# Kernel tuning notes

Hardware: AMD Instinct MI355X
Metric: run time of the kernel (lower is better)

The kernel has to match this reference:

```python
import jax, jax.numpy as jnp
import numpy as np

K = 15
LAM = 1.0
EPS = 1e-8


def _pdist(a):
    # pairwise euclidean distance (torch.cdist p=2), safe sqrt (zero grad at 0)
    sq = jnp.sum(a * a, axis=1)
    d2 = sq[:, None] + sq[None, :] - 2.0 * (a @ a.T)
    d2 = jnp.maximum(d2, 0.0)
    pos = d2 > 0
    return jnp.where(pos, jnp.sqrt(jnp.where(pos, d2, 1.0)), 0.0)


def _knn_distance_loss(z, xf, k):
    B = xf.shape[0]
    x_dist = _pdist(xf)
    z_dist = _pdist(z)
    eye = jnp.eye(B, dtype=bool)
    x_noself = jnp.where(eye, jnp.inf, x_dist)
    # k smallest per row -> top_k of negated distances
    _, knn_idx = jax.lax.top_k(-x_noself, k)          # (B, k)
    rows = jnp.arange(B)[:, None]
    mask = jnp.zeros((B, B), dtype=bool).at[rows, knn_idx].set(True)
    mask = mask | mask.T                              # symmetric kNN mask
    x_m = jnp.where(mask, x_dist, 0.0)
    z_m = jnp.where(mask, z_dist, 0.0)
    x_norm = x_m / (jnp.max(x_m) + EPS)
    z_norm = z_m / (jnp.max(z_m) + EPS)
    diff2 = jnp.where(mask, (z_norm - x_norm) ** 2, 0.0)
    return diff2.sum() / mask.sum().astype(diff2.dtype)


def _forward(x, We1, be1, We2, be2, Wd1, bd1, Wd2, bd2):
    h = jax.nn.relu(x @ We1 + be1)
    z = h @ We2 + be2                                  # (B, latent)
    h2 = jax.nn.relu(z @ Wd1 + bd1)
    x_rec = h2 @ Wd2 + bd2
    rec_loss = jnp.mean((x_rec - x) ** 2)
    dist_loss = _knn_distance_loss(z, x.reshape(x.shape[0], -1), K)
    return rec_loss + LAM * dist_loss


def setup_inputs() -> dict:
    key = jax.random.key(0)
    ks = jax.random.split(key, 5)
    B, D, H, L = 8192, 1024, 512, 64
    s = 0.02
    return {
        "x": jax.random.normal(ks[0], (B, D), dtype=jnp.float32),
        "We1": jax.random.normal(ks[1], (D, H), dtype=jnp.float32) * s,
        "be1": jnp.zeros((H,), dtype=jnp.float32),
        "We2": jax.random.normal(ks[2], (H, L), dtype=jnp.float32) * s,
        "be2": jnp.zeros((L,), dtype=jnp.float32),
        "Wd1": jax.random.normal(ks[3], (L, H), dtype=jnp.float32) * s,
        "bd1": jnp.zeros((H,), dtype=jnp.float32),
        "Wd2": jax.random.normal(ks[4], (H, D), dtype=jnp.float32) * s,
        "bd2": jnp.zeros((D,), dtype=jnp.float32),
    }


def reference(x, We1, be1, We2, be2, Wd1, bd1, Wd2, bd2):
    return _forward(x, We1, be1, We2, be2, Wd1, bd1, Wd2, bd2)
```

## Files before the change

### kernel.cpp

```cpp
#include <hip/hip_runtime.h>

#define BB 8192
#define DD 1024
#define HH 512
#define LL 64
#define KNN 15
#define NT 64
#define NTILES 2080
#define NG1 256
#define NEDGE (BB * KNN)
#define NEBLK (NEDGE / 128)

typedef __attribute__((ext_vector_type(4))) float f32x4;
typedef __attribute__((ext_vector_type(8))) short s16x8;
typedef __attribute__((ext_vector_type(8))) unsigned short u16x8;
typedef __attribute__((ext_vector_type(4))) unsigned short u16x4;
typedef __attribute__((ext_vector_type(4))) _Float16 f16x4;

typedef s16x8 fragT;

__device__ __forceinline__ unsigned short f2bf(float f) {
  unsigned u = __float_as_uint(f);
  return (unsigned short)((u + 0x7fffu + ((u >> 16) & 1u)) >> 16);
}

__device__ __forceinline__ void gload16(const void* g, void* l) {
  __builtin_amdgcn_global_load_lds((const __attribute__((address_space(1))) unsigned int*)g,
                                   (__attribute__((address_space(3))) unsigned int*)l, 16, 0, 0);
}

__device__ __forceinline__ float unpack_d2(unsigned u) {
  _Float16 h = __builtin_bit_cast(_Float16, (unsigned short)(u >> 16));
  return (float)h;
}

__device__ __forceinline__ void ins15(unsigned (&l)[KNN], unsigned u) {
  if (u < l[KNN - 1]) {
    unsigned v = u;
#pragma unroll
    for (int p = 0; p < KNN; ++p) {
      unsigned lo = min(v, l[p]);
      unsigned hi = max(v, l[p]);
      l[p] = lo;
      v = hi;
    }
  }
}

__global__ void k_prep(const float* __restrict__ x, unsigned short* __restrict__ xb,
                       float* __restrict__ sqx,
                       const float* __restrict__ We1, const float* __restrict__ We2,
                       const float* __restrict__ Wd1, const float* __restrict__ Wd2,
                       unsigned short* __restrict__ Wt1, unsigned short* __restrict__ Wt2,
                       unsigned short* __restrict__ Wt3, unsigned short* __restrict__ Wt4) {
  __shared__ float ps[4];
  __shared__ unsigned short T[64][65];
  int b = blockIdx.x;
  int t = threadIdx.x;
  if (b < BB) {
    f32x4 v = *(const f32x4*)(x + (size_t)b * DD + t * 4);
    u16x4 o;
    float s = 0.f;
#pragma unroll
    for (int j = 0; j < 4; ++j) {
      float f = v[j];
      s += f * f;
      o[j] = f2bf(f);
    }
    *(u16x4*)(xb + (size_t)b * DD + t * 4) = o;
#pragma unroll
    for (int off = 32; off >= 1; off >>= 1) s += __shfl_down(s, off);
    if ((t & 63) == 0) ps[t >> 6] = s;
    __syncthreads();
    if (t == 0) sqx[b] = ps[0] + ps[1] + ps[2] + ps[3];
    return;
  }
  int c = b - BB;
  const float* W;
  unsigned short* Wt;
  int Kd, N, idx;
  if (c < 128)      { W = We1; Wt = Wt1; Kd = DD; N = HH; idx = c; }
  else if (c < 136) { W = We2; Wt = Wt2; Kd = HH; N = LL; idx = c - 128; }
  else if (c < 144) { W = Wd1; Wt = Wt3; Kd = LL; N = HH; idx = c - 136; }
  else              { W = Wd2; Wt = Wt4; Kd = HH; N = DD; idx = c - 144; }
  int nx = Kd >> 6;
  int k0 = (idx % nx) * 64, n0 = (idx / nx) * 64;
  int kr = t >> 4, nc = (t & 15) * 4;
#pragma unroll
  for (int q = 0; q < 4; ++q) {
    int k = kr + q * 16;
    f32x4 v = *(const f32x4*)(W + (size_t)(k0 + k) * N + n0 + nc);
#pragma unroll
    for (int j = 0; j < 4; ++j) T[nc + j][k] = f2bf(v[j]);
  }
  __syncthreads();
#pragma unroll
  for (int q = 0; q < 2; ++q) {
    int s = t + q * 256;
    int n = s >> 3, cc = (s & 7) * 8;
    u16x8 o;
#pragma unroll
    for (int j = 0; j < 8; ++j) o[j] = T[n][cc + j];
    *(u16x8*)(Wt + (size_t)(n0 + n) * Kd + k0 + cc) = o;
  }
}

template <int NF, int RELU, int FUSE, int STF32, int STBF>
__device__ __forceinline__ void mgemm_body(
    char* LB, int m0, int n0,
    const unsigned short* __restrict__ A, const unsigned short* __restrict__ Wt,
    const float* __restrict__ bias, unsigned short* __restrict__ Cb, float* __restrict__ Cf,
    const float* __restrict__ Xref, float* __restrict__ rec_sum, int N, int Kd) {
  unsigned short* At = (unsigned short*)LB;
  unsigned short* Bt = (unsigned short*)(LB + 16384);
  int t = threadIdx.x;
  int lane = t & 63, w = t >> 6;
  int wr = w >> 1, wc = w & 1;
  int wbase = w * 64;

  const unsigned short* pA[4];
  const unsigned short* pB[NF];
#pragma unroll
  for (int q = 0; q < 4; ++q) {
    int s = q * 256 + t;
    int r = s >> 3, g = s & 7;
    pA[q] = A + (size_t)(m0 + r) * Kd + (g ^ (r & 7)) * 8;
  }
#pragma unroll
  for (int q = 0; q < NF; ++q) {
    int s = q * 256 + t;
    int r = s >> 3, g = s & 7;
    pB[q] = Wt + (size_t)(n0 + r) * Kd + (g ^ (r & 7)) * 8;
  }

  int lrow = lane & 15;
  int klo = (lane >> 4) << 4;
  int sw = (lane & 7) << 4;

  f32x4 acc[4][NF] = {};

  int ksteps = Kd >> 6;
#pragma unroll
  for (int q = 0; q < 4; ++q) { gload16(pA[q], At + (q * 256 + wbase) * 8); pA[q] += 64; }
#pragma unroll
  for (int q = 0; q < NF; ++q) { gload16(pB[q], Bt + (q * 256 + wbase) * 8); pB[q] += 64; }

  for (int kt = 0; kt < ksteps; ++kt) {
    __syncthreads();
    fragT af[2][4], bf[2][NF];
#pragma unroll
    for (int kh = 0; kh < 2; ++kh) {
      int kbyte = ((kh << 6) | klo) ^ sw;
#pragma unroll
      for (int m = 0; m < 4; ++m)
        af[kh][m] = *(const fragT*)((const char*)At + (wr * 64 + m * 16 + lrow) * 128 + kbyte);
#pragma unroll
      for (int n = 0; n < NF; ++n)
        bf[kh][n] = *(const fragT*)((const char*)Bt + (wc * NF * 16 + n * 16 + lrow) * 128 + kbyte);
    }
    __syncthreads();
    if (kt + 1 < ksteps) {
#pragma unroll
      for (int q = 0; q < 4; ++q) { gload16(pA[q], At + (q * 256 + wbase) * 8); pA[q] += 64; }
#pragma unroll
      for (int q = 0; q < NF; ++q) { gload16(pB[q], Bt + (q * 256 + wbase) * 8); pB[q] += 64; }
    }
#pragma unroll
    for (int kh = 0; kh < 2; ++kh)
#pragma unroll
      for (int m = 0; m < 4; ++m)
#pragma unroll
        for (int n = 0; n < NF; ++n)
          acc[m][n] =
              __builtin_amdgcn_mfma_f32_16x16x32_bf16(af[kh][m], bf[kh][n], acc[m][n], 0, 0, 0);
  }

  float local = 0.f;
#pragma unroll
  for (int m = 0; m < 4; ++m) {
    int row0 = m0 + wr * 64 + m * 16 + ((lane >> 4) << 2);
#pragma unroll
    for (int n = 0; n < NF; ++n) {
      int col = n0 + wc * NF * 16 + n * 16 + lrow;
      float bv = bias[col];
      f32x4 a = acc[m][n];
#pragma unroll
      for (int j = 0; j < 4; ++j) {
        float c = a[j] + bv;
        if (RELU) c = fmaxf(c, 0.f);
        if (FUSE) {
          float xv = Xref[(size_t)(row0 + j) * N + col];
          float d = c - xv;
          local = fmaf(d, d, local);
        }
        if (STBF) Cb[(size_t)(row0 + j) * N + col] = f2bf(c);
        if (STF32) Cf[(size_t)(row0 + j) * N + col] = c;
      }
    }
  }
  if (FUSE) {
#pragma unroll
    for (int off = 32; off >= 1; off >>= 1) local += __shfl_down(local, off);
    __shared__ float rs[4];
    if ((t & 63) == 0) rs[t >> 6] = local;
    __syncthreads();
    if (t == 0) atomicAdd(rec_sum, rs[0] + rs[1] + rs[2] + rs[3]);
  }
}

template <int NF, int RELU, int FUSE, int STF32, int STBF>
__global__ __launch_bounds__(256) void k_mgemm(
    const unsigned short* __restrict__ A, const unsigned short* __restrict__ Wt,
    const float* __restrict__ bias, unsigned short* __restrict__ Cb, float* __restrict__ Cf,
    const float* __restrict__ Xref, float* __restrict__ rec_sum, int N, int Kd) {
  __shared__ __attribute__((aligned(16))) char LB[16384 + NF * 32 * 128];
  mgemm_body<NF, RELU, FUSE, STF32, STBF>(LB, blockIdx.y * 128, blockIdx.x * (NF * 32),
                                          A, Wt, bias, Cb, Cf, Xref, rec_sum, N, Kd);
}

__global__ __launch_bounds__(256, 3) void k_gram_topk(
    const unsigned short* __restrict__ xb, const float* __restrict__ sqx,
    unsigned* __restrict__ part,
    const unsigned short* __restrict__ Wt1, const float* __restrict__ be1,
    unsigned short* __restrict__ hb) {
  __shared__ __attribute__((aligned(16))) char LB[33792];

  int bid0 = blockIdx.x;
  if (bid0 < NG1) {
    mgemm_body<4, 1, 0, 0, 1>(LB, (bid0 >> 2) * 128, (bid0 & 3) * 128,
                              xb, Wt1, be1, hb, nullptr, nullptr, nullptr, HH, DD);
    return;
  }

  unsigned short* At = (unsigned short*)LB;
  unsigned short* Bt = (unsigned short*)(LB + 16384);
  char* Sf = LB;
  unsigned* scratch = (unsigned*)(LB + 16384);
  float* sqr = (float*)(LB + 32768);
  float* sqc = (float*)(LB + 33280);

  int g = bid0 - NG1;
  int k = g & 7, m = g >> 3;
  int nA = 6 + 4 * (61 - 4 * k);
  int b, mm;
  if (m < nA) { b = k; mm = m; }
  else        { b = 15 - k; mm = m - nA; }
  int ctl, j;
  if (mm < 6) {
    if (mm < 1)      { ctl = 0; j = mm; }
    else if (mm < 3) { ctl = 1; j = mm - 1; }
    else             { ctl = 2; j = mm - 3; }
  } else {
    ctl = 3 + ((mm - 6) >> 2);
    j = (mm - 6) & 3;
  }
  int rt = 4 * b + j;
  int ct = 4 * b + ctl;
  bool diag = (rt == ct);
  int r0 = rt * 128, c0 = ct * 128;

  int t = threadIdx.x;
  int lane = t & 63, w = t >> 6;
  int wr = w >> 1, wc = w & 1;
  int wbase = w * 64;

  if (t < 128) {
    sqr[t] = sqx[r0 + t];
    sqc[t] = sqx[c0 + t];
  }

  const unsigned short* pA[4];
  const unsigned short* pB[4];
#pragma unroll
  for (int q = 0; q < 4; ++q) {
    int s = q * 256 + t;
    int r = s >> 3, gg = s & 7;
    int kk = (gg ^ (r & 7)) * 8;
    pA[q] = xb + (size_t)(r0 + r) * DD + kk;
    pB[q] = xb + (size_t)(c0 + r) * DD + kk;
  }

  int lrow = lane & 15;
  int klo = (lane >> 4) << 4;
  int sw = (lane & 7) << 4;

  f32x4 acc[16] = {};

#pragma unroll
  for (int q = 0; q < 4; ++q) {
    gload16(pA[q], At + (q * 256 + wbase) * 8); pA[q] += 64;
    gload16(pB[q], Bt + (q * 256 + wbase) * 8); pB[q] += 64;
  }

  for (int kt = 0; kt < 16; ++kt) {
    __syncthreads();
    fragT af[2][4], bf[2][4];
#pragma unroll
    for (int kh = 0; kh < 2; ++kh) {
      int kbyte = ((kh << 6) | klo) ^ sw;
#pragma unroll
      for (int mq = 0; mq < 4; ++mq)
        af[kh][mq] = *(const fragT*)((const char*)At + (wr * 64 + mq * 16 + lrow) * 128 + kbyte);
#pragma unroll
      for (int n = 0; n < 4; ++n)
        bf[kh][n] = *(const fragT*)((const char*)Bt + (wc * 64 + n * 16 + lrow) * 128 + kbyte);
    }
    __syncthreads();
    if (kt < 15) {
#pragma unroll
      for (int q = 0; q < 4; ++q) {
        gload16(pA[q], At + (q * 256 + wbase) * 8); pA[q] += 64;
        gload16(pB[q], Bt + (q * 256 + wbase) * 8); pB[q] += 64;
      }
    }
#pragma unroll
    for (int kh = 0; kh < 2; ++kh)
#pragma unroll
      for (int mq = 0; mq < 4; ++mq)
#pragma unroll
        for (int n = 0; n < 4; ++n)
          acc[mq * 4 + n] = __builtin_amdgcn_mfma_f32_16x16x32_bf16(af[kh][mq], bf[kh][n],
                                                                   acc[mq * 4 + n], 0, 0, 0);
  }

  unsigned rowlist[KNN];
#pragma unroll
  for (int p = 0; p < KNN; ++p) rowlist[p] = 0xFFFFFFFFu;

  int scanrow = t & 127, side = t >> 7;

#pragma unroll
  for (int nh = 0; nh < 2; ++nh) {
    if (wc == nh) {
#pragma unroll
      for (int mq = 0; mq < 4; ++mq) {
        int row0 = wr * 64 + mq * 16 + ((lane >> 4) << 2);
        f32x4 sq4 = *(const f32x4*)&sqr[row0];
#pragma unroll
        for (int n = 0; n < 4; ++n) {
          int colL = n * 16 + lrow;
          float sc = sqc[nh * 64 + colL];
          f32x4 a = acc[mq * 4 + n];
          f16x4 hv;
#pragma unroll
          for (int r = 0; r < 4; ++r) {
            float d2 = fmaxf(sq4[r] + sc - 2.f * a[r], 0.f);
            if (diag && (row0 + r == nh * 64 + colL)) d2 = 60000.f;
            hv[r] = (_Float16)d2;
          }
          *(f16x4*)(Sf + colL * 256 + (((row0 * 2)) ^ ((colL & 31) << 3))) = hv;
        }
      }
    }
    __syncthreads();
    {
      int cbase = side * 32;
      int jbase = c0 + nh * 64;
      for (int cc = 0; cc < 32; cc += 4) {
        unsigned u[4];
#pragma unroll
        for (int q = 0; q < 4; ++q) {
          int colL = cbase + cc + q;
          unsigned bits = *(const unsigned short*)(Sf + colL * 256 +
                                                   ((scanrow * 2) ^ ((colL & 31) << 3)));
          u[q] = (bits << 16) | (unsigned)(jbase + colL);
        }
        unsigned m4 = min(min(u[0], u[1]), min(u[2], u[3]));
        if (m4 < rowlist[KNN - 1]) {
#pragma unroll
          for (int q = 0; q < 4; ++q) ins15(rowlist, u[q]);
        }
      }
    }
    if (!diag) {
      int c = t & 63, seg = t >> 6;
      unsigned collist[KNN];
#pragma unroll
      for (int p = 0; p < KNN; ++p) collist[p] = 0xFFFFFFFFu;
      for (int rq = 0; rq < 8; ++rq) {
        int r = seg * 32 + rq * 4;
        u16x4 v4 = *(const u16x4*)(Sf + c * 256 + ((r * 2) ^ ((c & 31) << 3)));
        unsigned u[4];
#pragma unroll
        for (int jj = 0; jj < 4; ++jj) u[jj] = ((unsigned)v4[jj] << 16) | (unsigned)(r0 + r + jj);
        unsigned m4 = min(min(u[0], u[1]), min(u[2], u[3]));
        if (m4 < collist[KNN - 1]) {
#pragma unroll
          for (int jj = 0; jj < 4; ++jj) ins15(collist, u[jj]);
        }
      }
      __syncthreads();
#pragma unroll
      for (int p = 0; p < KNN; ++p) scratch[(c * 4 + seg) * KNN + p] = collist[p];
      __syncthreads();
      if (t < 64) {
        unsigned fin[KNN];
#pragma unroll
        for (int p = 0; p < KNN; ++p) fin[p] = 0xFFFFFFFFu;
        for (int s = 0; s < 4; ++s)
#pragma unroll
          for (int p = 0; p < KNN; ++p) ins15(fin, scratch[(t * 4 + s) * KNN + p]);
        int jj = c0 + nh * 64 + t;
#pragma unroll
        for (int p = 0; p < KNN; ++p) part[((size_t)(rt * KNN + p)) * BB + jj] = fin[p];
      }
    }
    __syncthreads();
  }

#pragma unroll
  for (int p = 0; p < KNN; ++p) scratch[(scanrow * 2 + side) * KNN + p] = rowlist[p];
  __syncthreads();
  if (t < 128) {
    unsigned fin[KNN];
#pragma unroll
    for (int p = 0; p < KNN; ++p) fin[p] = 0xFFFFFFFFu;
    for (int s = 0; s < 2; ++s)
#pragma unroll
      for (int p = 0; p < KNN; ++p) ins15(fin, scratch[(t * 2 + s) * KNN + p]);
    int i = r0 + t;
#pragma unroll
    for (int p = 0; p < KNN; ++p) part[((size_t)(ct * KNN + p)) * BB + i] = fin[p];
  }
}

__global__ void k_merge1(const unsigned* __restrict__ part, unsigned* __restrict__ part2) {
  int gid = blockIdx.x * 256 + threadIdx.x;
  int s = gid >> 13, i = gid & 8191;
  unsigned l[KNN];
#pragma unroll
  for (int p = 0; p < KNN; ++p) l[p] = 0xFFFFFFFFu;
  for (int b = s * 16; b < s * 16 + 16; ++b) {
    size_t base = (size_t)(b * KNN) * BB + i;
    unsigned u = part[base];
    if (u < l[KNN - 1]) {
      ins15(l, u);
      for (int p = 1; p < KNN; ++p) {
        u = part[base + (size_t)p * BB];
        if (u >= l[KNN - 1]) break;
        ins15(l, u);
      }
    }
  }
#pragma unroll
  for (int p = 0; p < KNN; ++p) part2[((size_t)(s * KNN + p)) * BB + i] = l[p];
}

__global__ void k_merge2(const unsigned* __restrict__ part2, float* __restrict__ knn_d2,
                         int* __restrict__ knn_idx, int* __restrict__ xmax_bits) {
  int i = blockIdx.x * 256 + threadIdx.x;
  unsigned l[KNN];
#pragma unroll
  for (int p = 0; p < KNN; ++p) l[p] = 0xFFFFFFFFu;
  for (int q = 0; q < 4; ++q) {
    size_t base = (size_t)(q * KNN) * BB + i;
    unsigned u = part2[base];
    if (u < l[KNN - 1]) {
      ins15(l, u);
      for (int p = 1; p < KNN; ++p) {
        u = part2[base + (size_t)p * BB];
        if (u >= l[KNN - 1]) break;
        ins15(l, u);
      }
    }
  }
  float mx = 0.f;
#pragma unroll
  for (int p = 0; p < KNN; ++p) {
    unsigned u = l[p];
    float d = fmaxf(unpack_d2(u), 0.f);
    mx = fmaxf(mx, d);
    knn_d2[(size_t)i * KNN + p] = d;
    knn_idx[(size_t)i * KNN + p] = (int)(u & 0xFFFFu);
  }
  int t = threadIdx.x;
#pragma unroll
  for (int off = 32; off >= 1; off >>= 1) mx = fmaxf(mx, __shfl_down(mx, off));
  __shared__ float rm[4];
  if ((t & 63) == 0) rm[t >> 6] = mx;
  __syncthreads();
  if (t == 0) {
    float mb = fmaxf(fmaxf(rm[0], rm[1]), fmaxf(rm[2], rm[3]));
    atomicMax(xmax_bits, __float_as_int(mb));
  }
}

__global__ void k_edge(const float* __restrict__ z, const int* __restrict__ knn_idx,
                       const float* __restrict__ knn_d2, float* __restrict__ pzz,
                       float* __restrict__ pxx, float* __restrict__ pxz,
                       float* __restrict__ pcnt, float* __restrict__ pzm) {
  int t = threadIdx.x;
  int g = t >> 4, L = t & 15;
  int lane = t & 63;
  float szz = 0.f, sxx = 0.f, sxz = 0.f, scnt = 0.f, zm = 0.f;
#pragma unroll
  for (int pass = 0; pass < 8; ++pass) {
    int e = blockIdx.x * 128 + pass * 16 + g;
    int i = e / KNN;
    int j = knn_idx[e];
    f32x4 zi = *(const f32x4*)(z + (size_t)i * LL + L * 4);
    f32x4 zj = *(const f32x4*)(z + (size_t)j * LL + L * 4);
    float v = 0.f;
#pragma unroll
    for (int d = 0; d < 4; ++d) {
      float df = zi[d] - zj[d];
      v = fmaf(df, df, v);
    }
    v += __shfl_down(v, 8);
    v += __shfl_down(v, 4);
    v += __shfl_down(v, 2);
    v += __shfl_down(v, 1);
    int cand = (L < KNN) ? knn_idx[(size_t)j * KNN + L] : -1;
    unsigned long long ball = __ballot(cand == i);
    unsigned recip = (unsigned)(ball >> (lane & 48)) & 0xFFFFu;
    if (L == 0) {
      float w = recip ? 1.f : 2.f;
      float xd2 = knn_d2[e];
      szz = fmaf(w, v, szz);
      sxx = fmaf(w, xd2, sxx);
      sxz = fmaf(w, sqrtf(v * xd2), sxz);
      scnt += w;
      zm = fmaxf(zm, v);
    }
  }
#pragma unroll
  for (int off = 32; off >= 1; off >>= 1) {
    szz += __shfl_down(szz, off);
    sxx += __shfl_down(sxx, off);
    sxz += __shfl_down(sxz, off);
    scnt += __shfl_down(scnt, off);
    zm = fmaxf(zm, __shfl_down(zm, off));
  }
  __shared__ float r[5][4];
  int w4 = t >> 6;
  if (lane == 0) {
    r[0][w4] = szz; r[1][w4] = sxx; r[2][w4] = sxz; r[3][w4] = scnt; r[4][w4] = zm;
  }
  __syncthreads();
  if (t == 0) {
    pzz[blockIdx.x] = r[0][0] + r[0][1] + r[0][2] + r[0][3];
    pxx[blockIdx.x] = r[1][0] + r[1][1] + r[1][2] + r[1][3];
    pxz[blockIdx.x] = r[2][0] + r[2][1] + r[2][2] + r[2][3];
    pcnt[blockIdx.x] = r[3][0] + r[3][1] + r[3][2] + r[3][3];
    pzm[blockIdx.x] = fmaxf(fmaxf(r[4][0], r[4][1]), fmaxf(r[4][2], r[4][3]));
  }
}

__global__ void k_final(const float* __restrict__ pzz, const float* __restrict__ pxx,
                        const float* __restrict__ pxz, const float* __restrict__ pcnt,
                        const float* __restrict__ pzm, const int* __restrict__ xmax_bits,
                        const float* __restrict__ rec_sum, float* __restrict__ out) {
  int t = threadIdx.x;
  float szz = 0.f, sxx = 0.f, sxz = 0.f, scnt = 0.f, zm = 0.f;
  for (int bb = t; bb < NEBLK; bb += 256) {
    szz += pzz[bb];
    sxx += pxx[bb];
    sxz += pxz[bb];
    scnt += pcnt[bb];
    zm = fmaxf(zm, pzm[bb]);
  }
#pragma unroll
  for (int off = 32; off >= 1; off >>= 1) {
    szz += __shfl_down(szz, off);
    sxx += __shfl_down(sxx, off);
    sxz += __shfl_down(sxz, off);
    scnt += __shfl_down(scnt, off);
    zm = fmaxf(zm, __shfl_down(zm, off));
  }
  __shared__ float r[5][4];
  int w4 = t >> 6;
  if ((t & 63) == 0) {
    r[0][w4] = szz; r[1][w4] = sxx; r[2][w4] = sxz; r[3][w4] = scnt; r[4][w4] = zm;
  }
  __syncthreads();
  if (t == 0) {
    float SZZ = r[0][0] + r[0][1] + r[0][2] + r[0][3];
    float SXX = r[1][0] + r[1][1] + r[1][2] + r[1][3];
    float SXZ = r[2][0] + r[2][1] + r[2][2] + r[2][3];
    float CNT = r[3][0] + r[3][1] + r[3][2] + r[3][3];
    float ZM = fmaxf(fmaxf(r[4][0], r[4][1]), fmaxf(r[4][2], r[4][3]));
    float xmax = __int_as_float(*xmax_bits);
    float a = 1.f / (sqrtf(ZM) + 1e-8f);
    float bq = 1.f / (sqrtf(xmax) + 1e-8f);
    float loss = (a * a * SZZ + bq * bq * SXX - 2.f * a * bq * SXZ) / CNT;
    out[0] = rec_sum[0] * (1.f / 8388608.f) + loss;
  }
}

extern "C" void kernel_launch(void* const* d_in, const int* in_sizes, int n_in,
                              void* d_out, int out_size, void* d_ws, size_t ws_size,
                              hipStream_t stream) {
  const float* x = (const float*)d_in[0];
  const float* We1 = (const float*)d_in[1];
  const float* be1 = (const float*)d_in[2];
  const float* We2 = (const float*)d_in[3];
  const float* be2 = (const float*)d_in[4];
  const float* Wd1 = (const float*)d_in[5];
  const float* bd1 = (const float*)d_in[6];
  const float* Wd2 = (const float*)d_in[7];
  const float* bd2 = (const float*)d_in[8];

  char* ws = (char*)d_ws;
  size_t off = 0;
  auto alloc = [&](size_t bytes) {
    void* p = ws + off;
    off += (bytes + 255) & ~(size_t)255;
    return p;
  };
  unsigned short* xb = (unsigned short*)alloc((size_t)BB * DD * 2);
  unsigned short* hb = (unsigned short*)alloc((size_t)BB * HH * 2);
  unsigned short* zb = (unsigned short*)alloc((size_t)BB * LL * 2);
  unsigned short* h2b = (unsigned short*)alloc((size_t)BB * HH * 2);
  float* z = (float*)alloc((size_t)BB * LL * 4);
  float* sqx = (float*)alloc((size_t)BB * 4);
  unsigned short* Wt1 = (unsigned short*)alloc((size_t)HH * DD * 2);
  unsigned short* Wt2 = (unsigned short*)alloc((size_t)LL * HH * 2);
  unsigned short* Wt3 = (unsigned short*)alloc((size_t)HH * LL * 2);
  unsigned short* Wt4 = (unsigned short*)alloc((size_t)DD * HH * 2);
  unsigned* part = (unsigned*)alloc((size_t)NT * KNN * BB * 4);
  unsigned* part2 = (unsigned*)alloc((size_t)4 * KNN * BB * 4);
  float* knn_d2 = (float*)alloc((size_t)BB * KNN * 4);
  int* knn_idx = (int*)alloc((size_t)BB * KNN * 4);
  float* pzz = (float*)alloc(NEBLK * 4);
  float* pxx = (float*)alloc(NEBLK * 4);
  float* pxz = (float*)alloc(NEBLK * 4);
  float* pcnt = (float*)alloc(NEBLK * 4);
  float* pzm = (float*)alloc(NEBLK * 4);
  float* scal = (float*)alloc(64);
  float* rec_sum = scal + 0;
  int* xmax_bits = (int*)(scal + 1);

  hipMemsetAsync(scal, 0, 64, stream);

  k_prep<<<BB + 272, 256, 0, stream>>>(x, xb, sqx, We1, We2, Wd1, Wd2, Wt1, Wt2, Wt3, Wt4);

  k_gram_topk<<<NG1 + NTILES, 256, 0, stream>>>(xb, sqx, part, Wt1, be1, hb);

  k_mgemm<2, 0, 0, 1, 1><<<dim3(LL / 64, BB / 128), 256, 0, stream>>>(
      hb, Wt2, be2, zb, z, nullptr, nullptr, LL, HH);
  k_mgemm<4, 1, 0, 0, 1><<<dim3(HH / 128, BB / 128), 256, 0, stream>>>(
      zb, Wt3, bd1, h2b, nullptr, nullptr, nullptr, HH, LL);
  k_mgemm<4, 0, 1, 0, 0><<<dim3(DD / 128, BB / 128), 256, 0, stream>>>(
      h2b, Wt4, bd2, nullptr, nullptr, x, rec_sum, DD, HH);

  k_merge1<<<128, 256, 0, stream>>>(part, part2);
  k_merge2<<<BB / 256, 256, 0, stream>>>(part2, knn_d2, knn_idx, xmax_bits);
  k_edge<<<NEBLK, 256, 0, stream>>>(z, knn_idx, knn_d2, pzz, pxx, pxz, pcnt, pzm);
  k_final<<<1, 256, 0, stream>>>(pzz, pxx, pxz, pcnt, pzm, xmax_bits, rec_sum, (float*)d_out);
}
```

Measured before the change: 321.5 us.

## Co-schedule tail GEMMs with kNN merge and edge kernels in combined launches

Six sequential tail kernels become three combined launches. Each launch pairs a decoder/latent GEMM with the independent kNN stage (merge1, merge2, edge) by splitting on block index, so the small merge and edge stages overlap with GEMM blocks. This removes three kernel launches and their serialization gaps. The cost is larger shared memory per block for the merge and edge blocks, and branch-divergent kernels whose occupancy is set by the GEMM path.

```diff
diff --git a/kernel.cpp b/kernel.cpp
--- a/kernel.cpp
+++ b/kernel.cpp
@@ -208,16 +208,6 @@
   }
 }
 
-template <int NF, int RELU, int FUSE, int STF32, int STBF>
-__global__ __launch_bounds__(256) void k_mgemm(
-    const unsigned short* __restrict__ A, const unsigned short* __restrict__ Wt,
-    const float* __restrict__ bias, unsigned short* __restrict__ Cb, float* __restrict__ Cf,
-    const float* __restrict__ Xref, float* __restrict__ rec_sum, int N, int Kd) {
-  __shared__ __attribute__((aligned(16))) char LB[16384 + NF * 32 * 128];
-  mgemm_body<NF, RELU, FUSE, STF32, STBF>(LB, blockIdx.y * 128, blockIdx.x * (NF * 32),
-                                          A, Wt, bias, Cb, Cf, Xref, rec_sum, N, Kd);
-}
-
 __global__ __launch_bounds__(256, 3) void k_gram_topk(
     const unsigned short* __restrict__ xb, const float* __restrict__ sqx,
     unsigned* __restrict__ part,
@@ -424,8 +414,8 @@
   }
 }
 
-__global__ void k_merge1(const unsigned* __restrict__ part, unsigned* __restrict__ part2) {
-  int gid = blockIdx.x * 256 + threadIdx.x;
+__device__ __forceinline__ void merge1_body(int gid, const unsigned* __restrict__ part,
+                                            unsigned* __restrict__ part2) {
   int s = gid >> 13, i = gid & 8191;
   unsigned l[KNN];
 #pragma unroll
@@ -446,9 +436,9 @@
   for (int p = 0; p < KNN; ++p) part2[((size_t)(s * KNN + p)) * BB + i] = l[p];
 }
 
-__global__ void k_merge2(const unsigned* __restrict__ part2, float* __restrict__ knn_d2,
-                         int* __restrict__ knn_idx, int* __restrict__ xmax_bits) {
-  int i = blockIdx.x * 256 + threadIdx.x;
+__device__ __forceinline__ void merge2_body(int i, const unsigned* __restrict__ part2,
+                                            float* __restrict__ knn_d2, int* __restrict__ knn_idx,
+                                            int* __restrict__ xmax_bits) {
   unsigned l[KNN];
 #pragma unroll
   for (int p = 0; p < KNN; ++p) l[p] = 0xFFFFFFFFu;
@@ -485,17 +475,19 @@
   }
 }
 
-__global__ void k_edge(const float* __restrict__ z, const int* __restrict__ knn_idx,
-                       const float* __restrict__ knn_d2, float* __restrict__ pzz,
-                       float* __restrict__ pxx, float* __restrict__ pxz,
-                       float* __restrict__ pcnt, float* __restrict__ pzm) {
+__device__ __forceinline__ void edge_body(int eb, const float* __restrict__ z,
+                                          const int* __restrict__ knn_idx,
+                                          const float* __restrict__ knn_d2,
+                                          float* __restrict__ pzz, float* __restrict__ pxx,
+                                          float* __restrict__ pxz, float* __restrict__ pcnt,
+                                          float* __restrict__ pzm) {
   int t = threadIdx.x;
   int g = t >> 4, L = t & 15;
   int lane = t & 63;
   float szz = 0.f, sxx = 0.f, sxz = 0.f, scnt = 0.f, zm = 0.f;
 #pragma unroll
   for (int pass = 0; pass < 8; ++pass) {
-    int e = blockIdx.x * 128 + pass * 16 + g;
+    int e = eb * 128 + pass * 16 + g;
     int i = e / KNN;
     int j = knn_idx[e];
     f32x4 zi = *(const f32x4*)(z + (size_t)i * LL + L * 4);
@@ -538,11 +530,55 @@
   }
   __syncthreads();
   if (t == 0) {
-    pzz[blockIdx.x] = r[0][0] + r[0][1] + r[0][2] + r[0][3];
-    pxx[blockIdx.x] = r[1][0] + r[1][1] + r[1][2] + r[1][3];
-    pxz[blockIdx.x] = r[2][0] + r[2][1] + r[2][2] + r[2][3];
-    pcnt[blockIdx.x] = r[3][0] + r[3][1] + r[3][2] + r[3][3];
-    pzm[blockIdx.x] = fmaxf(fmaxf(r[4][0], r[4][1]), fmaxf(r[4][2], r[4][3]));
+    pzz[eb] = r[0][0] + r[0][1] + r[0][2] + r[0][3];
+    pxx[eb] = r[1][0] + r[1][1] + r[1][2] + r[1][3];
+    pxz[eb] = r[2][0] + r[2][1] + r[2][2] + r[2][3];
+    pcnt[eb] = r[3][0] + r[3][1] + r[3][2] + r[3][3];
+    pzm[eb] = fmaxf(fmaxf(r[4][0], r[4][1]), fmaxf(r[4][2], r[4][3]));
+  }
+}
+
+__global__ __launch_bounds__(256) void k_tail2(
+    const unsigned short* __restrict__ hb, const unsigned short* __restrict__ Wt2,
+    const float* __restrict__ be2, unsigned short* __restrict__ zb, float* __restrict__ z,
+    const unsigned* __restrict__ part, unsigned* __restrict__ part2) {
+  __shared__ __attribute__((aligned(16))) char LB[16384 + 8192];
+  int bid = blockIdx.x;
+  if (bid < 64) {
+    mgemm_body<2, 0, 0, 1, 1>(LB, bid * 128, 0, hb, Wt2, be2, zb, z, nullptr, nullptr, LL, HH);
+  } else {
+    merge1_body((bid - 64) * 256 + threadIdx.x, part, part2);
+  }
+}
+
+__global__ __launch_bounds__(256) void k_tail3(
+    const unsigned short* __restrict__ zb, const unsigned short* __restrict__ Wt3,
+    const float* __restrict__ bd1, unsigned short* __restrict__ h2b,
+    const unsigned* __restrict__ part2, float* __restrict__ knn_d2, int* __restrict__ knn_idx,
+    int* __restrict__ xmax_bits) {
+  __shared__ __attribute__((aligned(16))) char LB[16384 + 16384];
+  int bid = blockIdx.x;
+  if (bid < 256) {
+    mgemm_body<4, 1, 0, 0, 1>(LB, (bid >> 2) * 128, (bid & 3) * 128, zb, Wt3, bd1, h2b, nullptr,
+                              nullptr, nullptr, HH, LL);
+  } else {
+    merge2_body((bid - 256) * 256 + threadIdx.x, part2, knn_d2, knn_idx, xmax_bits);
+  }
+}
+
+__global__ __launch_bounds__(256) void k_tail4(
+    const unsigned short* __restrict__ h2b, const unsigned short* __restrict__ Wt4,
+    const float* __restrict__ bd2, const float* __restrict__ x, float* __restrict__ rec_sum,
+    const float* __restrict__ z, const int* __restrict__ knn_idx,
+    const float* __restrict__ knn_d2, float* __restrict__ pzz, float* __restrict__ pxx,
+    float* __restrict__ pxz, float* __restrict__ pcnt, float* __restrict__ pzm) {
+  __shared__ __attribute__((aligned(16))) char LB[16384 + 16384];
+  int bid = blockIdx.x;
+  if (bid < 512) {
+    mgemm_body<4, 0, 1, 0, 0>(LB, (bid >> 3) * 128, (bid & 7) * 128, h2b, Wt4, bd2, nullptr,
+                              nullptr, x, rec_sum, DD, HH);
+  } else {
+    edge_body(bid - 512, z, knn_idx, knn_d2, pzz, pxx, pxz, pcnt, pzm);
   }
 }
 
@@ -636,15 +672,9 @@
 
   k_gram_topk<<<NG1 + NTILES, 256, 0, stream>>>(xb, sqx, part, Wt1, be1, hb);
 
-  k_mgemm<2, 0, 0, 1, 1><<<dim3(LL / 64, BB / 128), 256, 0, stream>>>(
-      hb, Wt2, be2, zb, z, nullptr, nullptr, LL, HH);
-  k_mgemm<4, 1, 0, 0, 1><<<dim3(HH / 128, BB / 128), 256, 0, stream>>>(
-      zb, Wt3, bd1, h2b, nullptr, nullptr, nullptr, HH, LL);
-  k_mgemm<4, 0, 1, 0, 0><<<dim3(DD / 128, BB / 128), 256, 0, stream>>>(
-      h2b, Wt4, bd2, nullptr, nullptr, x, rec_sum, DD, HH);
-
-  k_merge1<<<128, 256, 0, stream>>>(part, part2);
-  k_merge2<<<BB / 256, 256, 0, stream>>>(part2, knn_d2, knn_idx, xmax_bits);
-  k_edge<<<NEBLK, 256, 0, stream>>>(z, knn_idx, knn_d2, pzz, pxx, pxz, pcnt, pzm);
+  k_tail2<<<64 + 128, 256, 0, stream>>>(hb, Wt2, be2, zb, z, part, part2);
+  k_tail3<<<256 + 32, 256, 0, stream>>>(zb, Wt3, bd1, h2b, part2, knn_d2, knn_idx, xmax_bits);
+  k_tail4<<<512 + NEBLK, 256, 0, stream>>>(h2b, Wt4, bd2, x, rec_sum, z, knn_idx, knn_d2,
+                                           pzz, pxx, pxz, pcnt, pzm);
   k_final<<<1, 256, 0, stream>>>(pzz, pxx, pxz, pcnt, pzm, xmax_bits, rec_sum, (float*)d_out);
 }
```

Measured after the change: 330.8 us. 1.03x slower.
